# Optimization experiments

Measured on AMD Instinct MI355X. Metric: run time of the kernel, lower is better.

Reference implementation:

```python
import jax, jax.numpy as jnp
import numpy as np

VOCAB_SIZE = 32000


def setup_inputs() -> dict:
    key = jax.random.key(0)
    k1, k2, k3, k4 = jax.random.split(key, 4)
    B, S, T, H = 4, 512, 256, 1024
    return {
        "inputs": jax.random.randint(k1, (B, S), 0, VOCAB_SIZE, dtype=jnp.int32),
        "encoder_outputs": jax.random.normal(k2, (B, S, H), dtype=jnp.float32),
        "decoder_outputs": jax.random.normal(k3, (B, T, H), dtype=jnp.float32),
        "input_bias": jnp.zeros((B, S), dtype=jnp.float32),
        "W_proj": jax.random.normal(k4, (H, H), dtype=jnp.float32) * (1.0 / np.sqrt(H)),
        "b_proj": jnp.zeros((H,), dtype=jnp.float32),
    }


def reference(inputs, encoder_outputs, decoder_outputs, input_bias, W_proj, b_proj):
    # copy_projection: Dense(hidden) with tanh activation on encoder outputs
    enc = jnp.tanh(jnp.einsum("bsh,hk->bsk", encoder_outputs, W_proj) + b_proj)
    # decoder-encoder scores: [B, T, S]
    scores = jnp.einsum("bth,bsh->bts", decoder_outputs, enc)
    scores = scores + input_bias[:, None, :]  # bias broadcast over target dim
    probs = jax.nn.softmax(scores, axis=-1)  # [B, T, S]

    # map_updates_to_vocab: scatter-add probs into vocab slots by token id
    def scatter_one(p, ids):  # p: [T, S], ids: [S]
        return jnp.zeros((p.shape[0], VOCAB_SIZE), p.dtype).at[:, ids].add(p)

    copy_probs = jax.vmap(scatter_one)(probs, inputs)  # [B, T, V]
    return copy_probs
```

## Files before the change

### kernel.cpp

```cpp
#include <hip/hip_runtime.h>
#include <hip/hip_bf16.h>
#include <math.h>

typedef __bf16 bf16x8 __attribute__((ext_vector_type(8)));
typedef float  f32x4  __attribute__((ext_vector_type(4)));

__device__ __forceinline__ unsigned short f2bf(float x) {
    unsigned u = __float_as_uint(x);
    u += 0x7fffu + ((u >> 16) & 1u);
    return (unsigned short)(u >> 16);
}
__device__ __forceinline__ float bf2f(unsigned short h) {
    return __uint_as_float(((unsigned)h) << 16);
}

__device__ __forceinline__ void gl2lds16(const void* g, void* l) {
    __builtin_amdgcn_global_load_lds(
        (const __attribute__((address_space(1))) unsigned int*)(uintptr_t)g,
        (__attribute__((address_space(3))) unsigned int*)(unsigned int)(uintptr_t)l,
        16, 0, 0);
}

__global__ __launch_bounds__(256) void convert_split(const float* __restrict__ encf,
                                                     unsigned short* __restrict__ eh,
                                                     unsigned short* __restrict__ el,
                                                     const float* __restrict__ decf,
                                                     unsigned short* __restrict__ dh,
                                                     unsigned short* __restrict__ dl) {
    const int bid = blockIdx.x;
    const float* src; unsigned short *ph, *pl; int i;
    if (bid < 2048) { src = encf; ph = eh; pl = el; i = bid * 256 + threadIdx.x; }
    else            { src = decf; ph = dh; pl = dl; i = (bid - 2048) * 256 + threadIdx.x; }
    const float4 v = ((const float4*)src)[i];
    ushort4 h, l;
    h.x = f2bf(v.x); l.x = f2bf(v.x - bf2f(h.x));
    h.y = f2bf(v.y); l.y = f2bf(v.y - bf2f(h.y));
    h.z = f2bf(v.z); l.z = f2bf(v.z - bf2f(h.z));
    h.w = f2bf(v.w); l.w = f2bf(v.w - bf2f(h.w));
    ((ushort4*)ph)[i] = h;
    ((ushort4*)pl)[i] = l;
}

__global__ __launch_bounds__(256) void transpose_convert(const float* __restrict__ W,
                                                         unsigned short* __restrict__ Wth,
                                                         unsigned short* __restrict__ Wtl) {
    __shared__ float tile[64][65];
    const int k0 = blockIdx.y * 64, n0 = blockIdx.x * 64;
    const int c = threadIdx.x & 63, r0 = threadIdx.x >> 6;
    #pragma unroll
    for (int p = 0; p < 16; ++p) {
        int r = r0 + p * 4;
        tile[r][c] = W[(size_t)(k0 + r) * 1024 + n0 + c];
    }
    __syncthreads();
    #pragma unroll
    for (int p = 0; p < 16; ++p) {
        int rn = r0 + p * 4;
        float v = tile[c][rn];
        unsigned short h = f2bf(v);
        size_t idx = (size_t)(n0 + rn) * 1024 + k0 + c;
        Wth[idx] = h;
        Wtl[idx] = f2bf(v - bf2f(h));
    }
}

template <int EPI>
__global__ __launch_bounds__(256) void gemm_bt(
    const unsigned short* __restrict__ Ah, const unsigned short* __restrict__ Al,
    const unsigned short* __restrict__ Bh, const unsigned short* __restrict__ Bl,
    const float* __restrict__ bias,
    float* __restrict__ Cf, unsigned short* __restrict__ Ch, unsigned short* __restrict__ Cl,
    int N, int K, int kIter, int ksplit,
    long long aBatch, long long bBatch, long long cBatch, long long cPart) {

    const int z = blockIdx.z;
    const int batch = z / ksplit;
    const int ks = z - batch * ksplit;
    Ah += (size_t)batch * aBatch;  Al += (size_t)batch * aBatch;
    Bh += (size_t)batch * bBatch;  Bl += (size_t)batch * bBatch;
    const int kOff = ks * kIter * 64;

    __shared__ __align__(16) unsigned short sAh[64 * 64];
    __shared__ __align__(16) unsigned short sAl[64 * 64];
    __shared__ __align__(16) unsigned short sBh[64 * 64];
    __shared__ __align__(16) unsigned short sBl[64 * 64];

    const int t = threadIdx.x;
    const int lane = t & 63;
    const int w = t >> 6;
    const int wm = w >> 1, wn = w & 1;
    const int ln15 = lane & 15, q4 = lane >> 4;

    const int row0 = blockIdx.y * 64;
    const int col0 = blockIdx.x * 64;

    const int c0 = w * 128 + lane;
    const int r0s = c0 >> 3, g0 = ((c0 & 7) ^ (r0s & 7)) * 8;
    const int c1 = c0 + 64;
    const int r1s = c1 >> 3, g1 = ((c1 & 7) ^ (r1s & 7)) * 8;
    const size_t a0 = (size_t)(row0 + r0s) * K + kOff + g0;
    const size_t a1 = (size_t)(row0 + r1s) * K + kOff + g1;
    const size_t b0 = (size_t)(col0 + r0s) * K + kOff + g0;
    const size_t b1 = (size_t)(col0 + r1s) * K + kOff + g1;

    f32x4 acc[2][2] = {};

    for (int kk = 0; kk < kIter; ++kk) {
        const int k0 = kk * 64;
        gl2lds16(Ah + a0 + k0, &sAh[c0 * 8]);
        gl2lds16(Ah + a1 + k0, &sAh[c1 * 8]);
        gl2lds16(Al + a0 + k0, &sAl[c0 * 8]);
        gl2lds16(Al + a1 + k0, &sAl[c1 * 8]);
        gl2lds16(Bh + b0 + k0, &sBh[c0 * 8]);
        gl2lds16(Bh + b1 + k0, &sBh[c1 * 8]);
        gl2lds16(Bl + b0 + k0, &sBl[c0 * 8]);
        gl2lds16(Bl + b1 + k0, &sBl[c1 * 8]);
        __syncthreads();

        #pragma unroll
        for (int kh = 0; kh < 2; ++kh) {
            bf16x8 ah[2], al[2], bh[2], bl[2];
            #pragma unroll
            for (int i = 0; i < 2; ++i) {
                int rr = wm * 32 + i * 16 + ln15;
                int off = rr * 64 + (((kh * 4 + q4) ^ (rr & 7)) * 8);
                ah[i] = *(const bf16x8*)&sAh[off];
                al[i] = *(const bf16x8*)&sAl[off];
            }
            #pragma unroll
            for (int j = 0; j < 2; ++j) {
                int rr = wn * 32 + j * 16 + ln15;
                int off = rr * 64 + (((kh * 4 + q4) ^ (rr & 7)) * 8);
                bh[j] = *(const bf16x8*)&sBh[off];
                bl[j] = *(const bf16x8*)&sBl[off];
            }
            #pragma unroll
            for (int i = 0; i < 2; ++i)
                #pragma unroll
                for (int j = 0; j < 2; ++j) {
                    acc[i][j] = __builtin_amdgcn_mfma_f32_16x16x32_bf16(ah[i], bh[j], acc[i][j], 0, 0, 0);
                    acc[i][j] = __builtin_amdgcn_mfma_f32_16x16x32_bf16(ah[i], bl[j], acc[i][j], 0, 0, 0);
                    acc[i][j] = __builtin_amdgcn_mfma_f32_16x16x32_bf16(al[i], bh[j], acc[i][j], 0, 0, 0);
                }
        }
        __syncthreads();
    }

    float* outp = Cf + (size_t)batch * cBatch + (size_t)ks * cPart;
    #pragma unroll
    for (int i = 0; i < 2; ++i)
        #pragma unroll
        for (int j = 0; j < 2; ++j) {
            int colg = col0 + wn * 32 + j * 16 + ln15;
            #pragma unroll
            for (int r = 0; r < 4; ++r) {
                int rowg = row0 + wm * 32 + i * 16 + q4 * 4 + r;
                if (EPI == 0) {
                    outp[(size_t)rowg * N + colg] = acc[i][j][r];
                } else {
                    float tv = tanhf(acc[i][j][r] + bias[colg]);
                    unsigned short h = f2bf(tv);
                    size_t idx = (size_t)rowg * N + colg;
                    Ch[idx] = h;
                    Cl[idx] = f2bf(tv - bf2f(h));
                }
            }
        }
}

__inline__ __device__ float waveReduceMax(float v) {
    #pragma unroll
    for (int off = 32; off > 0; off >>= 1) v = fmaxf(v, __shfl_down(v, off));
    return v;
}
__inline__ __device__ float waveReduceSum(float v) {
    #pragma unroll
    for (int off = 32; off > 0; off >>= 1) v += __shfl_down(v, off);
    return v;
}

__global__ __launch_bounds__(256) void softmax_scatter(const float* __restrict__ scores,
                                                       const int* __restrict__ tokens,
                                                       const float* __restrict__ ibias,
                                                       float* __restrict__ out) {
    const int row = blockIdx.x;
    const int b = row >> 8;
    const float* s0 = scores + (size_t)row * 512;
    const float* s1 = s0 + (size_t)4 * 256 * 512;
    const float* bi = ibias + (size_t)b * 512;
    const int* tok = tokens + (size_t)b * 512;
    float* o = out + (size_t)row * 32000;

    __shared__ float red[4];
    const int tid = threadIdx.x;
    const int wid = tid >> 6, lane = tid & 63;

    float v0 = s0[tid]       + s1[tid]       + bi[tid];
    float v1 = s0[tid + 256] + s1[tid + 256] + bi[tid + 256];

    float m = fmaxf(v0, v1);
    m = waveReduceMax(m);
    if (lane == 0) red[wid] = m;
    __syncthreads();
    if (tid == 0) red[0] = fmaxf(fmaxf(red[0], red[1]), fmaxf(red[2], red[3]));
    __syncthreads();
    const float rowmax = red[0];
    __syncthreads();

    float e0 = __expf(v0 - rowmax);
    float e1 = __expf(v1 - rowmax);
    float s = e0 + e1;
    s = waveReduceSum(s);
    if (lane == 0) red[wid] = s;
    __syncthreads();
    if (tid == 0) red[0] = red[0] + red[1] + red[2] + red[3];
    __syncthreads();
    const float inv = 1.0f / red[0];

    float4 z = make_float4(0.f, 0.f, 0.f, 0.f);
    float4* o4 = (float4*)o;
    for (int i = tid; i < 8000; i += 256) o4[i] = z;

    __threadfence_block();
    __syncthreads();

    atomicAdd(&o[tok[tid]],       e0 * inv);
    atomicAdd(&o[tok[tid + 256]], e1 * inv);
}

extern "C" void kernel_launch(void* const* d_in, const int* in_sizes, int n_in,
                              void* d_out, int out_size, void* d_ws, size_t ws_size,
                              hipStream_t stream) {
    const int*   inputs  = (const int*)d_in[0];
    const float* enc_in  = (const float*)d_in[1];
    const float* dec_in  = (const float*)d_in[2];
    const float* ibias   = (const float*)d_in[3];
    const float* W       = (const float*)d_in[4];
    const float* bproj   = (const float*)d_in[5];
    float* out = (float*)d_out;

    float* scores = (float*)d_ws;

    size_t outBytes = (size_t)out_size * sizeof(float);
    unsigned short* tail = (unsigned short*)((char*)d_out + outBytes - (size_t)24 * 1024 * 1024);
    unsigned short* Aeh = tail;
    unsigned short* Ael = Aeh + (size_t)2048 * 1024;
    unsigned short* Dh  = Ael + (size_t)2048 * 1024;
    unsigned short* Dl  = Dh  + (size_t)1024 * 1024;
    unsigned short* Wth = Dl  + (size_t)1024 * 1024;
    unsigned short* Wtl = Wth + (size_t)1024 * 1024;
    unsigned short* ench = Wtl + (size_t)1024 * 1024;
    unsigned short* encl = ench + (size_t)2048 * 1024;

    convert_split<<<dim3(3072), 256, 0, stream>>>(enc_in, Aeh, Ael, dec_in, Dh, Dl);

    transpose_convert<<<dim3(16, 16), 256, 0, stream>>>(W, Wth, Wtl);

    gemm_bt<1><<<dim3(16, 32, 1), 256, 0, stream>>>(
        Aeh, Ael, Wth, Wtl, bproj, nullptr, ench, encl,
        1024, 1024, 16, 1, 0LL, 0LL, 0LL, 0LL);

    gemm_bt<0><<<dim3(8, 4, 8), 256, 0, stream>>>(
        Dh, Dl, ench, encl, nullptr, scores, nullptr, nullptr,
        512, 1024, 8, 2,
        (long long)256 * 1024, (long long)512 * 1024,
        (long long)256 * 512, (long long)4 * 256 * 512);

    softmax_scatter<<<dim3(4 * 256), 256, 0, stream>>>(scores, inputs, ibias, out);
}
```

Measured before the change: 209.7 us.

## Split-K both GEMMs and move tanh epilogue into a separate combine kernel

The projection GEMM now runs split-K by two, writing fp32 partials, and a new elementwise kernel sums them, adds the bias, applies tanh and splits the result into bf16 hi/lo. The scores GEMM goes from split-K 2 to 4, and the softmax kernel sums four partial planes. The aim is more workgroups to fill the GPU's compute units, since the projection GEMM had only 512 blocks. The cost is extra fp32 partial traffic, one more kernel launch, and 16 MB more scratch carved from the output buffer tail. The launch bound also gains a min-blocks hint of 4.

```diff
diff --git a/kernel.cpp b/kernel.cpp
--- a/kernel.cpp
+++ b/kernel.cpp
@@ -64,12 +64,10 @@
     }
 }
 
-template <int EPI>
-__global__ __launch_bounds__(256) void gemm_bt(
+__global__ __launch_bounds__(256, 4) void gemm_bt(
     const unsigned short* __restrict__ Ah, const unsigned short* __restrict__ Al,
     const unsigned short* __restrict__ Bh, const unsigned short* __restrict__ Bl,
-    const float* __restrict__ bias,
-    float* __restrict__ Cf, unsigned short* __restrict__ Ch, unsigned short* __restrict__ Cl,
+    float* __restrict__ Cf,
     int N, int K, int kIter, int ksplit,
     long long aBatch, long long bBatch, long long cBatch, long long cPart) {
 
@@ -155,17 +153,32 @@
             #pragma unroll
             for (int r = 0; r < 4; ++r) {
                 int rowg = row0 + wm * 32 + i * 16 + q4 * 4 + r;
-                if (EPI == 0) {
-                    outp[(size_t)rowg * N + colg] = acc[i][j][r];
-                } else {
-                    float tv = tanhf(acc[i][j][r] + bias[colg]);
-                    unsigned short h = f2bf(tv);
-                    size_t idx = (size_t)rowg * N + colg;
-                    Ch[idx] = h;
-                    Cl[idx] = f2bf(tv - bf2f(h));
-                }
+                outp[(size_t)rowg * N + colg] = acc[i][j][r];
             }
         }
+}
+
+__global__ __launch_bounds__(256) void tanh_combine(const float* __restrict__ P0,
+                                                    const float* __restrict__ P1,
+                                                    const float* __restrict__ bias,
+                                                    unsigned short* __restrict__ Ch,
+                                                    unsigned short* __restrict__ Cl) {
+    const int i = blockIdx.x * 256 + threadIdx.x;
+    const float4 p0 = ((const float4*)P0)[i];
+    const float4 p1 = ((const float4*)P1)[i];
+    const float4 bv = ((const float4*)bias)[i & 255];
+    float4 v;
+    v.x = tanhf(p0.x + p1.x + bv.x);
+    v.y = tanhf(p0.y + p1.y + bv.y);
+    v.z = tanhf(p0.z + p1.z + bv.z);
+    v.w = tanhf(p0.w + p1.w + bv.w);
+    ushort4 h, l;
+    h.x = f2bf(v.x); l.x = f2bf(v.x - bf2f(h.x));
+    h.y = f2bf(v.y); l.y = f2bf(v.y - bf2f(h.y));
+    h.z = f2bf(v.z); l.z = f2bf(v.z - bf2f(h.z));
+    h.w = f2bf(v.w); l.w = f2bf(v.w - bf2f(h.w));
+    ((ushort4*)Ch)[i] = h;
+    ((ushort4*)Cl)[i] = l;
 }
 
 __inline__ __device__ float waveReduceMax(float v) {
@@ -185,8 +198,8 @@
                                                        float* __restrict__ out) {
     const int row = blockIdx.x;
     const int b = row >> 8;
+    const size_t plane = (size_t)4 * 256 * 512;
     const float* s0 = scores + (size_t)row * 512;
-    const float* s1 = s0 + (size_t)4 * 256 * 512;
     const float* bi = ibias + (size_t)b * 512;
     const int* tok = tokens + (size_t)b * 512;
     float* o = out + (size_t)row * 32000;
@@ -195,8 +208,12 @@
     const int tid = threadIdx.x;
     const int wid = tid >> 6, lane = tid & 63;
 
-    float v0 = s0[tid]       + s1[tid]       + bi[tid];
-    float v1 = s0[tid + 256] + s1[tid + 256] + bi[tid + 256];
+    float v0 = bi[tid], v1 = bi[tid + 256];
+    #pragma unroll
+    for (int p = 0; p < 4; ++p) {
+        v0 += s0[p * plane + tid];
+        v1 += s0[p * plane + tid + 256];
+    }
 
     float m = fmaxf(v0, v1);
     m = waveReduceMax(m);
@@ -242,8 +259,8 @@
     float* scores = (float*)d_ws;
 
     size_t outBytes = (size_t)out_size * sizeof(float);
-    unsigned short* tail = (unsigned short*)((char*)d_out + outBytes - (size_t)24 * 1024 * 1024);
-    unsigned short* Aeh = tail;
+    char* tail = (char*)d_out + outBytes - (size_t)40 * 1024 * 1024;
+    unsigned short* Aeh = (unsigned short*)tail;
     unsigned short* Ael = Aeh + (size_t)2048 * 1024;
     unsigned short* Dh  = Ael + (size_t)2048 * 1024;
     unsigned short* Dl  = Dh  + (size_t)1024 * 1024;
@@ -251,18 +268,22 @@
     unsigned short* Wtl = Wth + (size_t)1024 * 1024;
     unsigned short* ench = Wtl + (size_t)1024 * 1024;
     unsigned short* encl = ench + (size_t)2048 * 1024;
+    float* P0 = (float*)(encl + (size_t)2048 * 1024);
+    float* P1 = P0 + (size_t)2048 * 1024;
 
     convert_split<<<dim3(3072), 256, 0, stream>>>(enc_in, Aeh, Ael, dec_in, Dh, Dl);
 
     transpose_convert<<<dim3(16, 16), 256, 0, stream>>>(W, Wth, Wtl);
 
-    gemm_bt<1><<<dim3(16, 32, 1), 256, 0, stream>>>(
-        Aeh, Ael, Wth, Wtl, bproj, nullptr, ench, encl,
-        1024, 1024, 16, 1, 0LL, 0LL, 0LL, 0LL);
-
-    gemm_bt<0><<<dim3(8, 4, 8), 256, 0, stream>>>(
-        Dh, Dl, ench, encl, nullptr, scores, nullptr, nullptr,
-        512, 1024, 8, 2,
+    gemm_bt<<<dim3(16, 32, 2), 256, 0, stream>>>(
+        Aeh, Ael, Wth, Wtl, P0,
+        1024, 1024, 8, 2, 0LL, 0LL, 0LL, (long long)2048 * 1024);
+
+    tanh_combine<<<dim3(2048), 256, 0, stream>>>(P0, P1, bproj, ench, encl);
+
+    gemm_bt<<<dim3(8, 4, 16), 256, 0, stream>>>(
+        Dh, Dl, ench, encl, scores,
+        512, 1024, 4, 4,
         (long long)256 * 1024, (long long)512 * 1024,
         (long long)256 * 512, (long long)4 * 256 * 512);
 
```

New measurement: 209.4 us. No clear change (-0.1%).

## Enlarge GEMM tiles to 128x128, merge prep kernels, raise split-K to four

Applied to the files above, without the earlier changes.

Both split-bf16 GEMMs now use 128x128 output tiles with a K step of 32 instead of 64x64 tiles with a K step of 64. The LDS swizzle and the per-wave fragment loads are reworked to match. This raises MFMA work per LDS load and cuts redundant global traffic. The encoder/decoder convert and the W transpose-convert are merged into one launch. The score GEMM moves from split-K 2 to 4, so softmax now sums four partial planes. The larger tiles shrink both GEMM grids to 128 blocks, which may leave many CUs idle, and the extra split-K plane doubles the scores workspace and its read traffic.

```diff
diff --git a/kernel.cpp b/kernel.cpp
--- a/kernel.cpp
+++ b/kernel.cpp
@@ -21,31 +21,33 @@
         16, 0, 0);
 }
 
-__global__ __launch_bounds__(256) void convert_split(const float* __restrict__ encf,
-                                                     unsigned short* __restrict__ eh,
-                                                     unsigned short* __restrict__ el,
-                                                     const float* __restrict__ decf,
-                                                     unsigned short* __restrict__ dh,
-                                                     unsigned short* __restrict__ dl) {
+__global__ __launch_bounds__(256) void prep(const float* __restrict__ encf,
+                                            unsigned short* __restrict__ eh,
+                                            unsigned short* __restrict__ el,
+                                            const float* __restrict__ decf,
+                                            unsigned short* __restrict__ dh,
+                                            unsigned short* __restrict__ dl,
+                                            const float* __restrict__ W,
+                                            unsigned short* __restrict__ Wth,
+                                            unsigned short* __restrict__ Wtl) {
     const int bid = blockIdx.x;
-    const float* src; unsigned short *ph, *pl; int i;
-    if (bid < 2048) { src = encf; ph = eh; pl = el; i = bid * 256 + threadIdx.x; }
-    else            { src = decf; ph = dh; pl = dl; i = (bid - 2048) * 256 + threadIdx.x; }
-    const float4 v = ((const float4*)src)[i];
-    ushort4 h, l;
-    h.x = f2bf(v.x); l.x = f2bf(v.x - bf2f(h.x));
-    h.y = f2bf(v.y); l.y = f2bf(v.y - bf2f(h.y));
-    h.z = f2bf(v.z); l.z = f2bf(v.z - bf2f(h.z));
-    h.w = f2bf(v.w); l.w = f2bf(v.w - bf2f(h.w));
-    ((ushort4*)ph)[i] = h;
-    ((ushort4*)pl)[i] = l;
-}
-
-__global__ __launch_bounds__(256) void transpose_convert(const float* __restrict__ W,
-                                                         unsigned short* __restrict__ Wth,
-                                                         unsigned short* __restrict__ Wtl) {
+    if (bid < 3072) {
+        const float* src; unsigned short *ph, *pl; int i;
+        if (bid < 2048) { src = encf; ph = eh; pl = el; i = bid * 256 + threadIdx.x; }
+        else            { src = decf; ph = dh; pl = dl; i = (bid - 2048) * 256 + threadIdx.x; }
+        const float4 v = ((const float4*)src)[i];
+        ushort4 h, l;
+        h.x = f2bf(v.x); l.x = f2bf(v.x - bf2f(h.x));
+        h.y = f2bf(v.y); l.y = f2bf(v.y - bf2f(h.y));
+        h.z = f2bf(v.z); l.z = f2bf(v.z - bf2f(h.z));
+        h.w = f2bf(v.w); l.w = f2bf(v.w - bf2f(h.w));
+        ((ushort4*)ph)[i] = h;
+        ((ushort4*)pl)[i] = l;
+        return;
+    }
     __shared__ float tile[64][65];
-    const int k0 = blockIdx.y * 64, n0 = blockIdx.x * 64;
+    const int tb = bid - 3072;
+    const int k0 = (tb >> 4) * 64, n0 = (tb & 15) * 64;
     const int c = threadIdx.x & 63, r0 = threadIdx.x >> 6;
     #pragma unroll
     for (int p = 0; p < 16; ++p) {
@@ -65,7 +67,7 @@
 }
 
 template <int EPI>
-__global__ __launch_bounds__(256) void gemm_bt(
+__global__ __launch_bounds__(256) void gemm128(
     const unsigned short* __restrict__ Ah, const unsigned short* __restrict__ Al,
     const unsigned short* __restrict__ Bh, const unsigned short* __restrict__ Bl,
     const float* __restrict__ bias,
@@ -78,12 +80,12 @@
     const int ks = z - batch * ksplit;
     Ah += (size_t)batch * aBatch;  Al += (size_t)batch * aBatch;
     Bh += (size_t)batch * bBatch;  Bl += (size_t)batch * bBatch;
-    const int kOff = ks * kIter * 64;
-
-    __shared__ __align__(16) unsigned short sAh[64 * 64];
-    __shared__ __align__(16) unsigned short sAl[64 * 64];
-    __shared__ __align__(16) unsigned short sBh[64 * 64];
-    __shared__ __align__(16) unsigned short sBl[64 * 64];
+    const int kOff = ks * kIter * 32;
+
+    __shared__ __align__(16) unsigned short sAh[128 * 32];
+    __shared__ __align__(16) unsigned short sAl[128 * 32];
+    __shared__ __align__(16) unsigned short sBh[128 * 32];
+    __shared__ __align__(16) unsigned short sBl[128 * 32];
 
     const int t = threadIdx.x;
     const int lane = t & 63;
@@ -91,22 +93,22 @@
     const int wm = w >> 1, wn = w & 1;
     const int ln15 = lane & 15, q4 = lane >> 4;
 
-    const int row0 = blockIdx.y * 64;
-    const int col0 = blockIdx.x * 64;
-
-    const int c0 = w * 128 + lane;
-    const int r0s = c0 >> 3, g0 = ((c0 & 7) ^ (r0s & 7)) * 8;
-    const int c1 = c0 + 64;
-    const int r1s = c1 >> 3, g1 = ((c1 & 7) ^ (r1s & 7)) * 8;
+    const int row0 = blockIdx.y * 128;
+    const int col0 = blockIdx.x * 128;
+
+    const int c0 = t,        r0s = c0 >> 2, g0 = ((c0 & 3) ^ (r0s & 3) ^ ((r0s >> 2) & 3)) * 8;
+    const int c1 = t + 256,  r1s = c1 >> 2, g1 = ((c1 & 3) ^ (r1s & 3) ^ ((r1s >> 2) & 3)) * 8;
     const size_t a0 = (size_t)(row0 + r0s) * K + kOff + g0;
     const size_t a1 = (size_t)(row0 + r1s) * K + kOff + g1;
     const size_t b0 = (size_t)(col0 + r0s) * K + kOff + g0;
     const size_t b1 = (size_t)(col0 + r1s) * K + kOff + g1;
 
-    f32x4 acc[2][2] = {};
+    const int pq = (q4 ^ (ln15 & 3) ^ ((ln15 >> 2) & 3)) * 8;
+
+    f32x4 acc[4][4] = {};
 
     for (int kk = 0; kk < kIter; ++kk) {
-        const int k0 = kk * 64;
+        const int k0 = kk * 32;
         gl2lds16(Ah + a0 + k0, &sAh[c0 * 8]);
         gl2lds16(Ah + a1 + k0, &sAh[c1 * 8]);
         gl2lds16(Al + a0 + k0, &sAl[c0 * 8]);
@@ -117,48 +119,44 @@
         gl2lds16(Bl + b1 + k0, &sBl[c1 * 8]);
         __syncthreads();
 
-        #pragma unroll
-        for (int kh = 0; kh < 2; ++kh) {
-            bf16x8 ah[2], al[2], bh[2], bl[2];
+        bf16x8 ah[4], al[4], bh[4], bl[4];
+        #pragma unroll
+        for (int i = 0; i < 4; ++i) {
+            int rr = wm * 64 + i * 16 + ln15;
+            ah[i] = *(const bf16x8*)&sAh[rr * 32 + pq];
+            al[i] = *(const bf16x8*)&sAl[rr * 32 + pq];
+        }
+        #pragma unroll
+        for (int j = 0; j < 4; ++j) {
+            int rr = wn * 64 + j * 16 + ln15;
+            bh[j] = *(const bf16x8*)&sBh[rr * 32 + pq];
+            bl[j] = *(const bf16x8*)&sBl[rr * 32 + pq];
+        }
+        #pragma unroll
+        for (int i = 0; i < 4; ++i)
             #pragma unroll
-            for (int i = 0; i < 2; ++i) {
-                int rr = wm * 32 + i * 16 + ln15;
-                int off = rr * 64 + (((kh * 4 + q4) ^ (rr & 7)) * 8);
-                ah[i] = *(const bf16x8*)&sAh[off];
-                al[i] = *(const bf16x8*)&sAl[off];
+            for (int j = 0; j < 4; ++j) {
+                acc[i][j] = __builtin_amdgcn_mfma_f32_16x16x32_bf16(ah[i], bh[j], acc[i][j], 0, 0, 0);
+                acc[i][j] = __builtin_amdgcn_mfma_f32_16x16x32_bf16(ah[i], bl[j], acc[i][j], 0, 0, 0);
+                acc[i][j] = __builtin_amdgcn_mfma_f32_16x16x32_bf16(al[i], bh[j], acc[i][j], 0, 0, 0);
             }
-            #pragma unroll
-            for (int j = 0; j < 2; ++j) {
-                int rr = wn * 32 + j * 16 + ln15;
-                int off = rr * 64 + (((kh * 4 + q4) ^ (rr & 7)) * 8);
-                bh[j] = *(const bf16x8*)&sBh[off];
-                bl[j] = *(const bf16x8*)&sBl[off];
-            }
-            #pragma unroll
-            for (int i = 0; i < 2; ++i)
-                #pragma unroll
-                for (int j = 0; j < 2; ++j) {
-                    acc[i][j] = __builtin_amdgcn_mfma_f32_16x16x32_bf16(ah[i], bh[j], acc[i][j], 0, 0, 0);
-                    acc[i][j] = __builtin_amdgcn_mfma_f32_16x16x32_bf16(ah[i], bl[j], acc[i][j], 0, 0, 0);
-                    acc[i][j] = __builtin_amdgcn_mfma_f32_16x16x32_bf16(al[i], bh[j], acc[i][j], 0, 0, 0);
-                }
-        }
         __syncthreads();
     }
 
-    float* outp = Cf + (size_t)batch * cBatch + (size_t)ks * cPart;
-    #pragma unroll
-    for (int i = 0; i < 2; ++i)
-        #pragma unroll
-        for (int j = 0; j < 2; ++j) {
-            int colg = col0 + wn * 32 + j * 16 + ln15;
+    float* outp = (EPI == 0) ? (Cf + (size_t)batch * cBatch + (size_t)ks * cPart) : nullptr;
+    #pragma unroll
+    for (int i = 0; i < 4; ++i)
+        #pragma unroll
+        for (int j = 0; j < 4; ++j) {
+            int colg = col0 + wn * 64 + j * 16 + ln15;
+            float bv = (EPI == 1) ? bias[colg] : 0.0f;
             #pragma unroll
             for (int r = 0; r < 4; ++r) {
-                int rowg = row0 + wm * 32 + i * 16 + q4 * 4 + r;
+                int rowg = row0 + wm * 64 + i * 16 + q4 * 4 + r;
                 if (EPI == 0) {
                     outp[(size_t)rowg * N + colg] = acc[i][j][r];
                 } else {
-                    float tv = tanhf(acc[i][j][r] + bias[colg]);
+                    float tv = tanhf(acc[i][j][r] + bv);
                     unsigned short h = f2bf(tv);
                     size_t idx = (size_t)rowg * N + colg;
                     Ch[idx] = h;
@@ -185,8 +183,8 @@
                                                        float* __restrict__ out) {
     const int row = blockIdx.x;
     const int b = row >> 8;
+    const size_t plane = (size_t)4 * 256 * 512;
     const float* s0 = scores + (size_t)row * 512;
-    const float* s1 = s0 + (size_t)4 * 256 * 512;
     const float* bi = ibias + (size_t)b * 512;
     const int* tok = tokens + (size_t)b * 512;
     float* o = out + (size_t)row * 32000;
@@ -195,8 +193,12 @@
     const int tid = threadIdx.x;
     const int wid = tid >> 6, lane = tid & 63;
 
-    float v0 = s0[tid]       + s1[tid]       + bi[tid];
-    float v1 = s0[tid + 256] + s1[tid + 256] + bi[tid + 256];
+    float v0 = bi[tid], v1 = bi[tid + 256];
+    #pragma unroll
+    for (int p = 0; p < 4; ++p) {
+        v0 += s0[p * plane + tid];
+        v1 += s0[p * plane + tid + 256];
+    }
 
     float m = fmaxf(v0, v1);
     m = waveReduceMax(m);
@@ -242,8 +244,8 @@
     float* scores = (float*)d_ws;
 
     size_t outBytes = (size_t)out_size * sizeof(float);
-    unsigned short* tail = (unsigned short*)((char*)d_out + outBytes - (size_t)24 * 1024 * 1024);
-    unsigned short* Aeh = tail;
+    char* tail = (char*)d_out + outBytes - (size_t)24 * 1024 * 1024;
+    unsigned short* Aeh = (unsigned short*)tail;
     unsigned short* Ael = Aeh + (size_t)2048 * 1024;
     unsigned short* Dh  = Ael + (size_t)2048 * 1024;
     unsigned short* Dl  = Dh  + (size_t)1024 * 1024;
@@ -252,17 +254,15 @@
     unsigned short* ench = Wtl + (size_t)1024 * 1024;
     unsigned short* encl = ench + (size_t)2048 * 1024;
 
-    convert_split<<<dim3(3072), 256, 0, stream>>>(enc_in, Aeh, Ael, dec_in, Dh, Dl);
-
-    transpose_convert<<<dim3(16, 16), 256, 0, stream>>>(W, Wth, Wtl);
-
-    gemm_bt<1><<<dim3(16, 32, 1), 256, 0, stream>>>(
+    prep<<<dim3(3328), 256, 0, stream>>>(enc_in, Aeh, Ael, dec_in, Dh, Dl, W, Wth, Wtl);
+
+    gemm128<1><<<dim3(8, 16, 1), 256, 0, stream>>>(
         Aeh, Ael, Wth, Wtl, bproj, nullptr, ench, encl,
-        1024, 1024, 16, 1, 0LL, 0LL, 0LL, 0LL);
-
-    gemm_bt<0><<<dim3(8, 4, 8), 256, 0, stream>>>(
+        1024, 1024, 32, 1, 0LL, 0LL, 0LL, 0LL);
+
+    gemm128<0><<<dim3(4, 2, 16), 256, 0, stream>>>(
         Dh, Dl, ench, encl, nullptr, scores, nullptr, nullptr,
-        512, 1024, 8, 2,
+        512, 1024, 8, 4,
         (long long)256 * 1024, (long long)512 * 1024,
         (long long)256 * 512, (long long)4 * 256 * 512);
 
```

New measurement: 242.0 us. 15.4% more time.

## Switch split-bf16 GEMMs to two-term fp16 MFMA and fuse prep kernels

Applied to the files above, without the earlier changes.

Both GEMMs move from bf16 hi/lo splitting with three MFMAs to fp16 hi/lo splitting on the A operand only and two MFMAs. The B operands (transposed W and the encoder projection) are kept as a single fp16 value, which removes their lo buffers and LDS tiles. The split-convert and transpose kernels are merged into one launch, and the scores GEMM goes from split-K 2 to split-K 4, with softmax summing four partial planes. This cuts MFMA work, memory traffic and launch count. In exchange, precision is lower on B and fp16 range is limited for unnormalized inputs.

```diff
diff --git a/kernel.cpp b/kernel.cpp
--- a/kernel.cpp
+++ b/kernel.cpp
@@ -2,16 +2,16 @@
 #include <hip/hip_bf16.h>
 #include <math.h>
 
-typedef __bf16 bf16x8 __attribute__((ext_vector_type(8)));
-typedef float  f32x4  __attribute__((ext_vector_type(4)));
-
-__device__ __forceinline__ unsigned short f2bf(float x) {
-    unsigned u = __float_as_uint(x);
-    u += 0x7fffu + ((u >> 16) & 1u);
-    return (unsigned short)(u >> 16);
-}
-__device__ __forceinline__ float bf2f(unsigned short h) {
-    return __uint_as_float(((unsigned)h) << 16);
+typedef _Float16 f16x8 __attribute__((ext_vector_type(8)));
+typedef float    f32x4 __attribute__((ext_vector_type(4)));
+
+__device__ __forceinline__ unsigned short h2us(_Float16 v) {
+    return *(unsigned short*)&v;
+}
+__device__ __forceinline__ void f2h2(float x, unsigned short& hi, unsigned short& lo) {
+    _Float16 h = (_Float16)x;
+    _Float16 l = (_Float16)(x - (float)h);
+    hi = h2us(h); lo = h2us(l);
 }
 
 __device__ __forceinline__ void gl2lds16(const void* g, void* l) {
@@ -21,31 +21,32 @@
         16, 0, 0);
 }
 
-__global__ __launch_bounds__(256) void convert_split(const float* __restrict__ encf,
-                                                     unsigned short* __restrict__ eh,
-                                                     unsigned short* __restrict__ el,
-                                                     const float* __restrict__ decf,
-                                                     unsigned short* __restrict__ dh,
-                                                     unsigned short* __restrict__ dl) {
+__global__ __launch_bounds__(256) void prep(const float* __restrict__ encf,
+                                            unsigned short* __restrict__ eh,
+                                            unsigned short* __restrict__ el,
+                                            const float* __restrict__ decf,
+                                            unsigned short* __restrict__ dh,
+                                            unsigned short* __restrict__ dl,
+                                            const float* __restrict__ W,
+                                            unsigned short* __restrict__ Wth) {
     const int bid = blockIdx.x;
-    const float* src; unsigned short *ph, *pl; int i;
-    if (bid < 2048) { src = encf; ph = eh; pl = el; i = bid * 256 + threadIdx.x; }
-    else            { src = decf; ph = dh; pl = dl; i = (bid - 2048) * 256 + threadIdx.x; }
-    const float4 v = ((const float4*)src)[i];
-    ushort4 h, l;
-    h.x = f2bf(v.x); l.x = f2bf(v.x - bf2f(h.x));
-    h.y = f2bf(v.y); l.y = f2bf(v.y - bf2f(h.y));
-    h.z = f2bf(v.z); l.z = f2bf(v.z - bf2f(h.z));
-    h.w = f2bf(v.w); l.w = f2bf(v.w - bf2f(h.w));
-    ((ushort4*)ph)[i] = h;
-    ((ushort4*)pl)[i] = l;
-}
-
-__global__ __launch_bounds__(256) void transpose_convert(const float* __restrict__ W,
-                                                         unsigned short* __restrict__ Wth,
-                                                         unsigned short* __restrict__ Wtl) {
+    if (bid < 3072) {
+        const float* src; unsigned short *ph, *pl; int i;
+        if (bid < 2048) { src = encf; ph = eh; pl = el; i = bid * 256 + threadIdx.x; }
+        else            { src = decf; ph = dh; pl = dl; i = (bid - 2048) * 256 + threadIdx.x; }
+        const float4 v = ((const float4*)src)[i];
+        ushort4 h, l;
+        f2h2(v.x, h.x, l.x);
+        f2h2(v.y, h.y, l.y);
+        f2h2(v.z, h.z, l.z);
+        f2h2(v.w, h.w, l.w);
+        ((ushort4*)ph)[i] = h;
+        ((ushort4*)pl)[i] = l;
+        return;
+    }
     __shared__ float tile[64][65];
-    const int k0 = blockIdx.y * 64, n0 = blockIdx.x * 64;
+    const int tb = bid - 3072;
+    const int k0 = (tb >> 4) * 64, n0 = (tb & 15) * 64;
     const int c = threadIdx.x & 63, r0 = threadIdx.x >> 6;
     #pragma unroll
     for (int p = 0; p < 16; ++p) {
@@ -57,19 +58,17 @@
     for (int p = 0; p < 16; ++p) {
         int rn = r0 + p * 4;
         float v = tile[c][rn];
-        unsigned short h = f2bf(v);
-        size_t idx = (size_t)(n0 + rn) * 1024 + k0 + c;
-        Wth[idx] = h;
-        Wtl[idx] = f2bf(v - bf2f(h));
+        _Float16 h = (_Float16)v;
+        Wth[(size_t)(n0 + rn) * 1024 + k0 + c] = h2us(h);
     }
 }
 
 template <int EPI>
-__global__ __launch_bounds__(256) void gemm_bt(
+__global__ __launch_bounds__(256) void gemm_f16(
     const unsigned short* __restrict__ Ah, const unsigned short* __restrict__ Al,
-    const unsigned short* __restrict__ Bh, const unsigned short* __restrict__ Bl,
+    const unsigned short* __restrict__ Bh,
     const float* __restrict__ bias,
-    float* __restrict__ Cf, unsigned short* __restrict__ Ch, unsigned short* __restrict__ Cl,
+    float* __restrict__ Cf, unsigned short* __restrict__ Ch,
     int N, int K, int kIter, int ksplit,
     long long aBatch, long long bBatch, long long cBatch, long long cPart) {
 
@@ -77,13 +76,12 @@
     const int batch = z / ksplit;
     const int ks = z - batch * ksplit;
     Ah += (size_t)batch * aBatch;  Al += (size_t)batch * aBatch;
-    Bh += (size_t)batch * bBatch;  Bl += (size_t)batch * bBatch;
+    Bh += (size_t)batch * bBatch;
     const int kOff = ks * kIter * 64;
 
     __shared__ __align__(16) unsigned short sAh[64 * 64];
     __shared__ __align__(16) unsigned short sAl[64 * 64];
     __shared__ __align__(16) unsigned short sBh[64 * 64];
-    __shared__ __align__(16) unsigned short sBl[64 * 64];
 
     const int t = threadIdx.x;
     const int lane = t & 63;
@@ -113,56 +111,50 @@
         gl2lds16(Al + a1 + k0, &sAl[c1 * 8]);
         gl2lds16(Bh + b0 + k0, &sBh[c0 * 8]);
         gl2lds16(Bh + b1 + k0, &sBh[c1 * 8]);
-        gl2lds16(Bl + b0 + k0, &sBl[c0 * 8]);
-        gl2lds16(Bl + b1 + k0, &sBl[c1 * 8]);
         __syncthreads();
 
         #pragma unroll
         for (int kh = 0; kh < 2; ++kh) {
-            bf16x8 ah[2], al[2], bh[2], bl[2];
+            f16x8 ah[2], al[2], bh[2];
             #pragma unroll
             for (int i = 0; i < 2; ++i) {
                 int rr = wm * 32 + i * 16 + ln15;
                 int off = rr * 64 + (((kh * 4 + q4) ^ (rr & 7)) * 8);
-                ah[i] = *(const bf16x8*)&sAh[off];
-                al[i] = *(const bf16x8*)&sAl[off];
+                ah[i] = *(const f16x8*)&sAh[off];
+                al[i] = *(const f16x8*)&sAl[off];
             }
             #pragma unroll
             for (int j = 0; j < 2; ++j) {
                 int rr = wn * 32 + j * 16 + ln15;
                 int off = rr * 64 + (((kh * 4 + q4) ^ (rr & 7)) * 8);
-                bh[j] = *(const bf16x8*)&sBh[off];
-                bl[j] = *(const bf16x8*)&sBl[off];
+                bh[j] = *(const f16x8*)&sBh[off];
             }
             #pragma unroll
             for (int i = 0; i < 2; ++i)
                 #pragma unroll
                 for (int j = 0; j < 2; ++j) {
-                    acc[i][j] = __builtin_amdgcn_mfma_f32_16x16x32_bf16(ah[i], bh[j], acc[i][j], 0, 0, 0);
-                    acc[i][j] = __builtin_amdgcn_mfma_f32_16x16x32_bf16(ah[i], bl[j], acc[i][j], 0, 0, 0);
-                    acc[i][j] = __builtin_amdgcn_mfma_f32_16x16x32_bf16(al[i], bh[j], acc[i][j], 0, 0, 0);
+                    acc[i][j] = __builtin_amdgcn_mfma_f32_16x16x32_f16(ah[i], bh[j], acc[i][j], 0, 0, 0);
+                    acc[i][j] = __builtin_amdgcn_mfma_f32_16x16x32_f16(al[i], bh[j], acc[i][j], 0, 0, 0);
                 }
         }
         __syncthreads();
     }
 
-    float* outp = Cf + (size_t)batch * cBatch + (size_t)ks * cPart;
+    float* outp = (EPI == 0) ? (Cf + (size_t)batch * cBatch + (size_t)ks * cPart) : nullptr;
     #pragma unroll
     for (int i = 0; i < 2; ++i)
         #pragma unroll
         for (int j = 0; j < 2; ++j) {
             int colg = col0 + wn * 32 + j * 16 + ln15;
+            float bv = (EPI == 1) ? bias[colg] : 0.0f;
             #pragma unroll
             for (int r = 0; r < 4; ++r) {
                 int rowg = row0 + wm * 32 + i * 16 + q4 * 4 + r;
                 if (EPI == 0) {
                     outp[(size_t)rowg * N + colg] = acc[i][j][r];
                 } else {
-                    float tv = tanhf(acc[i][j][r] + bias[colg]);
-                    unsigned short h = f2bf(tv);
-                    size_t idx = (size_t)rowg * N + colg;
-                    Ch[idx] = h;
-                    Cl[idx] = f2bf(tv - bf2f(h));
+                    _Float16 h = (_Float16)tanhf(acc[i][j][r] + bv);
+                    Ch[(size_t)rowg * N + colg] = h2us(h);
                 }
             }
         }
@@ -185,8 +177,8 @@
                                                        float* __restrict__ out) {
     const int row = blockIdx.x;
     const int b = row >> 8;
+    const size_t plane = (size_t)4 * 256 * 512;
     const float* s0 = scores + (size_t)row * 512;
-    const float* s1 = s0 + (size_t)4 * 256 * 512;
     const float* bi = ibias + (size_t)b * 512;
     const int* tok = tokens + (size_t)b * 512;
     float* o = out + (size_t)row * 32000;
@@ -195,8 +187,12 @@
     const int tid = threadIdx.x;
     const int wid = tid >> 6, lane = tid & 63;
 
-    float v0 = s0[tid]       + s1[tid]       + bi[tid];
-    float v1 = s0[tid + 256] + s1[tid + 256] + bi[tid + 256];
+    float v0 = bi[tid], v1 = bi[tid + 256];
+    #pragma unroll
+    for (int p = 0; p < 4; ++p) {
+        v0 += s0[p * plane + tid];
+        v1 += s0[p * plane + tid + 256];
+    }
 
     float m = fmaxf(v0, v1);
     m = waveReduceMax(m);
@@ -242,27 +238,23 @@
     float* scores = (float*)d_ws;
 
     size_t outBytes = (size_t)out_size * sizeof(float);
-    unsigned short* tail = (unsigned short*)((char*)d_out + outBytes - (size_t)24 * 1024 * 1024);
-    unsigned short* Aeh = tail;
+    char* tail = (char*)d_out + outBytes - (size_t)20 * 1024 * 1024;
+    unsigned short* Aeh = (unsigned short*)tail;
     unsigned short* Ael = Aeh + (size_t)2048 * 1024;
     unsigned short* Dh  = Ael + (size_t)2048 * 1024;
     unsigned short* Dl  = Dh  + (size_t)1024 * 1024;
     unsigned short* Wth = Dl  + (size_t)1024 * 1024;
-    unsigned short* Wtl = Wth + (size_t)1024 * 1024;
-    unsigned short* ench = Wtl + (size_t)1024 * 1024;
-    unsigned short* encl = ench + (size_t)2048 * 1024;
-
-    convert_split<<<dim3(3072), 256, 0, stream>>>(enc_in, Aeh, Ael, dec_in, Dh, Dl);
-
-    transpose_convert<<<dim3(16, 16), 256, 0, stream>>>(W, Wth, Wtl);
-
-    gemm_bt<1><<<dim3(16, 32, 1), 256, 0, stream>>>(
-        Aeh, Ael, Wth, Wtl, bproj, nullptr, ench, encl,
+    unsigned short* ench = Wth + (size_t)1024 * 1024;
+
+    prep<<<dim3(3328), 256, 0, stream>>>(enc_in, Aeh, Ael, dec_in, Dh, Dl, W, Wth);
+
+    gemm_f16<1><<<dim3(16, 32, 1), 256, 0, stream>>>(
+        Aeh, Ael, Wth, bproj, nullptr, ench,
         1024, 1024, 16, 1, 0LL, 0LL, 0LL, 0LL);
 
-    gemm_bt<0><<<dim3(8, 4, 8), 256, 0, stream>>>(
-        Dh, Dl, ench, encl, nullptr, scores, nullptr, nullptr,
-        512, 1024, 8, 2,
+    gemm_f16<0><<<dim3(8, 4, 16), 256, 0, stream>>>(
+        Dh, Dl, ench, nullptr, scores, nullptr,
+        512, 1024, 4, 4,
         (long long)256 * 1024, (long long)512 * 1024,
         (long long)256 * 512, (long long)4 * 256 * 512);
 
```

Measured after the change: 202.3 us. 1.04x faster.
